# Kernel tuning notes

Measured on AMD Instinct MI355X. Metric: run time of the kernel, lower is better.

Reference implementation:

```python
import jax, jax.numpy as jnp
import numpy as np

B, S, EMBED, DK, DV, M = 8, 1024, 1024, 512, 512, 64


def setup_inputs() -> dict:
    key = jax.random.key(0)
    ks = jax.random.split(key, 9)
    query_in = jax.random.normal(ks[0], (B, S, EMBED), dtype=jnp.float32)
    key_in = jax.random.normal(ks[1], (B, S, EMBED), dtype=jnp.float32)
    value_in = jax.random.normal(ks[2], (B, S, EMBED), dtype=jnp.float32)
    lim = 1.0 / np.sqrt(EMBED)  # nn.Linear default init range
    u = lambda k, shape: jax.random.uniform(k, shape, minval=-lim, maxval=lim, dtype=jnp.float32)
    return {
        'query_in': query_in, 'key_in': key_in, 'value_in': value_in,
        'Wq': u(ks[3], (DK, EMBED)), 'bq': u(ks[4], (DK,)),
        'Wk': u(ks[5], (DK, EMBED)), 'bk': u(ks[6], (DK,)),
        'Wv': u(ks[7], (DV, EMBED)), 'bv': u(ks[8], (DV,)),
    }


def _select_landmarks(k_proj, m):
    # Original code runs recursive RLS sampling (random, host-side) over the m
    # segment-rows of key.reshape(B, m, seg, d) and gathers m of them back,
    # then flattens to (B, S, d). We use a deterministic data-dependent
    # selection (rows ranked by squared norm) with identical gather structure.
    Bb, Ss, d = k_proj.shape
    seg = Ss // m
    kr = k_proj.reshape(Bb, m, seg, d)
    scores = jnp.sum(kr * kr, axis=(2, 3))                      # [B, m]
    idx = jnp.argsort(-scores, axis=1)                          # [B, m]
    land = jnp.take_along_axis(kr, idx[:, :, None, None], axis=1)
    return land.reshape(Bb, Ss, d)                              # [B, S, d]


def reference(query_in, key_in, value_in, Wq, bq, Wk, bk, Wv, bv):
    scaling = DK ** -0.25  # 1/sqrt(sqrt(d_k)), applied to both q and k
    q = (jnp.einsum('bse,de->bsd', query_in, Wq) + bq) * scaling
    k = (jnp.einsum('bse,de->bsd', key_in, Wk) + bk) * scaling
    v = jnp.einsum('bse,de->bsd', value_in, Wv) + bv

    kl = _select_landmarks(k, M)                                # [B, S, DK]
    # is_decoder_self_attn is hard-coded True upstream -> q_landmarks = q,
    # so kernel_2 == kernel_1.
    kernel_1 = jax.nn.softmax(jnp.einsum('bqd,bkd->bqk', q, kl), axis=-1)
    kernel_2 = kernel_1
    kernel_3 = jax.nn.softmax(jnp.einsum('bqd,bkd->bqk', q, k), axis=-1)

    k2_inv = jnp.linalg.pinv(kernel_2)                          # [B, S, S] batched SVD
    out = jnp.einsum('bqk,bkd->bqd', jnp.einsum('bqm,bmk->bqk', kernel_1, k2_inv),
                     jnp.einsum('bqk,bkd->bqd', kernel_3, v))
    # dropout is identity in eval mode
    return out
```

## Files before the change

### kernel.cpp

```cpp
#include <hip/hip_runtime.h>
#include <hip/hip_bf16.h>

#define SS   1024
#define DKK  512

typedef __hip_bfloat16 bf16;
typedef __attribute__((ext_vector_type(8))) short s16x8;
typedef __attribute__((ext_vector_type(8))) unsigned short u16x8;
typedef __attribute__((ext_vector_type(4))) float f32x4;

#define WS_W(z)  ((48ull << 20) + ((size_t)(z) << 20))
#define WS_ST    (51ull << 20)
#define WS_Q     (52ull << 20)
#define WS_K     (60ull << 20)
#define WS_VT    (68ull << 20)
#define WS_LG    (0ull)

__device__ __forceinline__ void async_ld16(const void* g, void* s) {
  __builtin_amdgcn_global_load_lds(
      (const __attribute__((address_space(1))) void*)g,
      (__attribute__((address_space(3))) void*)s, 16, 0, 0);
}

__device__ __forceinline__ unsigned short f2bfu(float f) {
  return __builtin_bit_cast(unsigned short, __float2bfloat16(f));
}
__device__ __forceinline__ float bfu2f(unsigned short u) {
  unsigned int i = ((unsigned int)u) << 16;
  return __builtin_bit_cast(float, i);
}

__global__ __launch_bounds__(256)
void convert_w(const float* __restrict__ w0, const float* __restrict__ w1,
               const float* __restrict__ w2, char* __restrict__ ws)
{
  const int bx = blockIdx.x;
  const int z = bx >> 8, local = bx & 255;
  const float* src = (z == 0) ? w0 : (z == 1) ? w1 : w2;
  unsigned short* dst = (unsigned short*)(ws + WS_W(z));
  const int i = local * 2048 + threadIdx.x * 8;
  const float4* s = (const float4*)(src + i);
  float4 a = s[0], b = s[1];
  ushort4 o0, o1;
  o0.x = f2bfu(a.x); o0.y = f2bfu(a.y); o0.z = f2bfu(a.z); o0.w = f2bfu(a.w);
  o1.x = f2bfu(b.x); o1.y = f2bfu(b.y); o1.z = f2bfu(b.z); o1.w = f2bfu(b.w);
  ((ushort4*)(dst + i))[0] = o0;
  ((ushort4*)(dst + i))[1] = o1;
}

template<int BM, int K, int LDA, int LDB>
__device__ __forceinline__ void gemm_core(const bf16* __restrict__ A,
                                          const bf16* __restrict__ Bw,
                                          int bm, int bn,
                                          short* As, short* Bs, f32x4* acc)
{
  constexpr int MI = BM / 32;
  constexpr int AR = BM / 4;
  const int tid  = threadIdx.x;
  const int lane = tid & 63;
  const int wave = tid >> 6;
  const int l8   = lane >> 3;
  const int kch  = ((lane & 7) ^ l8) * 8;
  const bf16* ag = A  + (size_t)(bm * BM + wave * AR + l8) * LDA + kch;
  const bf16* bg = Bw + (size_t)(bn * 128 + wave * 32 + l8) * LDB + kch;
  short* AsW = As + wave * AR * 64;
  short* BsW = Bs + wave * 32 * 64;
  const int waveM = wave >> 1, waveN = wave & 1;
  const int l16  = lane & 15;
  const int quad = lane >> 4;
  const int xr   = l16 & 7;

  #pragma unroll
  for (int t = 0; t < MI * 4; ++t)
    #pragma unroll
    for (int r = 0; r < 4; ++r) acc[t][r] = 0.0f;

  for (int kt = 0; kt < K / 64; ++kt) {
    #pragma unroll
    for (int j = 0; j < AR / 8; ++j) async_ld16(ag + (size_t)j * 8 * LDA, AsW + j * 8 * 64);
    #pragma unroll
    for (int j = 0; j < 4; ++j)      async_ld16(bg + (size_t)j * 8 * LDB, BsW + j * 8 * 64);
    ag += 64; bg += 64;
    __syncthreads();
    #pragma unroll
    for (int ks = 0; ks < 2; ++ks) {
      s16x8 af[MI], bfv[4];
      #pragma unroll
      for (int mi = 0; mi < MI; ++mi) {
        const int row  = waveM * (BM / 2) + mi * 16 + l16;
        const int slot = (ks * 4 + quad) ^ xr;
        af[mi] = *(const s16x8*)&As[row * 64 + slot * 8];
      }
      #pragma unroll
      for (int ni = 0; ni < 4; ++ni) {
        const int row  = waveN * 64 + ni * 16 + l16;
        const int slot = (ks * 4 + quad) ^ xr;
        bfv[ni] = *(const s16x8*)&Bs[row * 64 + slot * 8];
      }
      #pragma unroll
      for (int mi = 0; mi < MI; ++mi)
        #pragma unroll
        for (int ni = 0; ni < 4; ++ni)
          acc[mi * 4 + ni] = __builtin_amdgcn_mfma_f32_16x16x32_bf16(
              af[mi], bfv[ni], acc[mi * 4 + ni], 0, 0, 0);
    }
    __syncthreads();
  }
}

template<int K, int LDA, int LDB>
__device__ __forceinline__ void gemm_core_f32a(const float* __restrict__ A,
                                               const bf16* __restrict__ Bw,
                                               int bm, int bn,
                                               short* As, short* Bs, f32x4* acc)
{
  const int tid  = threadIdx.x;
  const int lane = tid & 63;
  const int wave = tid >> 6;
  const int l8   = lane >> 3;
  const int kch  = ((lane & 7) ^ l8) * 8;
  const bf16* bg = Bw + (size_t)(bn * 256 + wave * 64 + l8) * LDB + kch;
  short* BsW = Bs + wave * 64 * 64;
  const int arow = tid >> 3;
  const int ag8  = tid & 7;
  const int slotA = (ag8 ^ (arow & 7)) * 8;
  const float* ag = A + (size_t)(bm * 64 + arow) * LDA + ag8 * 8;
  const int waveM = wave >> 1, waveN = wave & 1;
  const int l16  = lane & 15;
  const int quad = lane >> 4;
  const int xr   = l16 & 7;

  #pragma unroll
  for (int t = 0; t < 16; ++t)
    #pragma unroll
    for (int r = 0; r < 4; ++r) acc[t][r] = 0.0f;

  for (int kt = 0; kt < K / 64; ++kt) {
    #pragma unroll
    for (int j = 0; j < 8; ++j) async_ld16(bg + (size_t)j * 8 * LDB, BsW + j * 8 * 64);
    bg += 64;
    #pragma unroll
    for (int p = 0; p < 2; ++p) {
      const float4* s = (const float4*)(ag + (size_t)p * 32 * LDA);
      float4 a = s[0], b = s[1];
      u16x8 v;
      v[0] = f2bfu(a.x); v[1] = f2bfu(a.y); v[2] = f2bfu(a.z); v[3] = f2bfu(a.w);
      v[4] = f2bfu(b.x); v[5] = f2bfu(b.y); v[6] = f2bfu(b.z); v[7] = f2bfu(b.w);
      *(u16x8*)&As[(p * 32 + arow) * 64 + slotA] = v;
    }
    ag += 64;
    __syncthreads();
    #pragma unroll
    for (int ks = 0; ks < 2; ++ks) {
      s16x8 af[2], bfv[8];
      #pragma unroll
      for (int mi = 0; mi < 2; ++mi) {
        const int row  = waveM * 32 + mi * 16 + l16;
        const int slot = (ks * 4 + quad) ^ xr;
        af[mi] = *(const s16x8*)&As[row * 64 + slot * 8];
      }
      #pragma unroll
      for (int ni = 0; ni < 8; ++ni) {
        const int row  = waveN * 128 + ni * 16 + l16;
        const int slot = (ks * 4 + quad) ^ xr;
        bfv[ni] = *(const s16x8*)&Bs[row * 64 + slot * 8];
      }
      #pragma unroll
      for (int mi = 0; mi < 2; ++mi)
        #pragma unroll
        for (int ni = 0; ni < 8; ++ni)
          acc[mi * 8 + ni] = __builtin_amdgcn_mfma_f32_16x16x32_bf16(
              af[mi], bfv[ni], acc[mi * 8 + ni], 0, 0, 0);
    }
    __syncthreads();
  }
}

__global__ __launch_bounds__(256, 3)
void proj_kernel(const float* __restrict__ Xq, const float* __restrict__ Xk,
                 const float* __restrict__ Xv, const bf16* __restrict__ W0,
                 const float* __restrict__ bq, const float* __restrict__ bk,
                 const float* __restrict__ bv,
                 bf16* __restrict__ qo, bf16* __restrict__ ko,
                 bf16* __restrict__ vT, float qscale)
{
  __shared__ __align__(16) short As[64 * 64];
  __shared__ __align__(16) short Bs[256 * 64];
  const int id   = blockIdx.x;
  const int xcd  = id & 7;
  const int s    = id >> 3;
  const int bn   = s & 1;
  const int pair = (s >> 1) * 8 + xcd;
  const int bm   = pair & 127;
  const int z    = pair >> 7;
  const float* A  = (z == 0) ? Xq : (z == 1) ? Xk : Xv;
  const bf16*  Bw = W0 + ((size_t)z << 19);
  const float* bias = (z == 0) ? bq : (z == 1) ? bk : bv;
  f32x4 acc[16];
  gemm_core_f32a<1024, 1024, 1024>(A, Bw, bm, bn, As, Bs, acc);

  const int lane = threadIdx.x & 63;
  const int wave = threadIdx.x >> 6;
  const int waveM = wave >> 1, waveN = wave & 1;
  const int l16 = lane & 15, quad = lane >> 4;
  const int row0 = bm * 64 + waveM * 32;
  const int col0 = bn * 256 + waveN * 128;
  const float sc = (z == 0) ? qscale : 1.0f;
  bf16* C = (z == 0) ? qo : ko;
  #pragma unroll
  for (int ni = 0; ni < 8; ++ni) {
    const int col = col0 + ni * 16 + l16;
    const float bb = bias[col];
    #pragma unroll
    for (int mi = 0; mi < 2; ++mi)
      #pragma unroll
      for (int r = 0; r < 4; ++r) {
        const int row = row0 + mi * 16 + quad * 4 + r;
        const float v = acc[mi * 8 + ni][r] + bb;
        if (z == 2)
          vT[((size_t)(row >> 10) * DKK + col) * SS + (row & (SS - 1))] =
              __float2bfloat16(v);
        else
          C[(size_t)row * DKK + col] = __float2bfloat16(v * sc);
      }
  }
}

__global__ __launch_bounds__(256, 4)
void scores_kernel(const bf16* __restrict__ q, const bf16* __restrict__ k,
                   bf16* __restrict__ lgB, float* __restrict__ stats)
{
  __shared__ __align__(16) short As[64 * 64];
  __shared__ __align__(16) short Bs[128 * 64];
  const int z = blockIdx.z;
  const int bn = blockIdx.x, bm = blockIdx.y;
  f32x4 acc[8];
  gemm_core<64, 512, 512, 512>(q + (size_t)z * SS * DKK, k + (size_t)z * SS * DKK,
                               bm, bn, As, Bs, acc);

  const int lane = threadIdx.x & 63;
  const int wave = threadIdx.x >> 6;
  const int waveM = wave >> 1, waveN = wave & 1;
  const int l16 = lane & 15, quad = lane >> 4;
  const int row0 = bm * 64 + waveM * 32;
  const int col0 = bn * 128 + waveN * 64;
  bf16* C = lgB + (size_t)z * SS * SS;
  #pragma unroll
  for (int ni = 0; ni < 4; ++ni) {
    const int col = col0 + ni * 16 + l16;
    #pragma unroll
    for (int mi = 0; mi < 2; ++mi)
      #pragma unroll
      for (int r = 0; r < 4; ++r) {
        const int row = row0 + mi * 16 + quad * 4 + r;
        C[(size_t)row * SS + col] = __float2bfloat16(acc[mi * 4 + ni][r]);
      }
  }
  const int chunk = bn * 2 + waveN;
  #pragma unroll
  for (int mi = 0; mi < 2; ++mi)
    #pragma unroll
    for (int r = 0; r < 4; ++r) {
      float xr4[4];
      float m = -1e30f;
      #pragma unroll
      for (int ni = 0; ni < 4; ++ni) {
        xr4[ni] = bfu2f(f2bfu(acc[mi * 4 + ni][r]));
        m = fmaxf(m, xr4[ni]);
      }
      #pragma unroll
      for (int msk = 1; msk < 16; msk <<= 1) m = fmaxf(m, __shfl_xor(m, msk));
      float e = 0.f;
      #pragma unroll
      for (int ni = 0; ni < 4; ++ni) e += __expf(xr4[ni] - m);
      #pragma unroll
      for (int msk = 1; msk < 16; msk <<= 1) e += __shfl_xor(e, msk);
      if (l16 == 0) {
        const int row = row0 + mi * 16 + quad * 4 + r;
        float2 mr; mr.x = m; mr.y = e;
        *(float2*)&stats[(((size_t)z * SS + row) * 16 + chunk) * 2] = mr;
      }
    }
}

__device__ __forceinline__ void gemm_core_pv(const unsigned short* __restrict__ lg,
                                             const bf16* __restrict__ vT,
                                             int bm, int bn,
                                             const float* Ml, const float* Rl,
                                             short* As, short* Bs, f32x4* acc)
{
  const int tid  = threadIdx.x;
  const int lane = tid & 63;
  const int wave = tid >> 6;
  const int l8   = lane >> 3;
  const int kch  = ((lane & 7) ^ l8) * 8;
  const bf16* bg = vT + (size_t)(bn * 128 + wave * 32 + l8) * 1024 + kch;
  short* BsW = Bs + wave * 32 * 64;
  const int arow = tid >> 3;
  const int ag8  = tid & 7;
  const int slotA = (ag8 ^ (arow & 7)) * 8;
  const unsigned short* ag = lg + (size_t)(bm * 64 + arow) * 1024 + ag8 * 8;
  const int waveM = wave >> 1, waveN = wave & 1;
  const int l16  = lane & 15;
  const int quad = lane >> 4;
  const int xr   = l16 & 7;

  #pragma unroll
  for (int t = 0; t < 8; ++t)
    #pragma unroll
    for (int r = 0; r < 4; ++r) acc[t][r] = 0.0f;

  for (int kt = 0; kt < 16; ++kt) {
    #pragma unroll
    for (int j = 0; j < 4; ++j) async_ld16(bg + (size_t)j * 8 * 1024, BsW + j * 8 * 64);
    bg += 64;
    #pragma unroll
    for (int p = 0; p < 2; ++p) {
      const int rl = p * 32 + arow;
      u16x8 u = *(const u16x8*)(ag + (size_t)p * 32 * 1024);
      const float M = Ml[rl], R = Rl[rl];
      u16x8 v;
      #pragma unroll
      for (int j = 0; j < 8; ++j)
        v[j] = f2bfu(__expf(bfu2f((unsigned short)u[j]) - M) * R);
      *(u16x8*)&As[rl * 64 + slotA] = v;
    }
    ag += 64;
    __syncthreads();
    #pragma unroll
    for (int ks = 0; ks < 2; ++ks) {
      s16x8 af[2], bfv[4];
      #pragma unroll
      for (int mi = 0; mi < 2; ++mi) {
        const int row  = waveM * 32 + mi * 16 + l16;
        const int slot = (ks * 4 + quad) ^ xr;
        af[mi] = *(const s16x8*)&As[row * 64 + slot * 8];
      }
      #pragma unroll
      for (int ni = 0; ni < 4; ++ni) {
        const int row  = waveN * 64 + ni * 16 + l16;
        const int slot = (ks * 4 + quad) ^ xr;
        bfv[ni] = *(const s16x8*)&Bs[row * 64 + slot * 8];
      }
      #pragma unroll
      for (int mi = 0; mi < 2; ++mi)
        #pragma unroll
        for (int ni = 0; ni < 4; ++ni)
          acc[mi * 4 + ni] = __builtin_amdgcn_mfma_f32_16x16x32_bf16(
              af[mi], bfv[ni], acc[mi * 4 + ni], 0, 0, 0);
    }
    __syncthreads();
  }
}

__global__ __launch_bounds__(256, 4)
void pv_kernel(const unsigned short* __restrict__ lgB, const bf16* __restrict__ vT,
               const float* __restrict__ stats, float* __restrict__ out)
{
  __shared__ __align__(16) short As[64 * 64];
  __shared__ __align__(16) short Bs[128 * 64];
  __shared__ float Ml[64], Rl[64];
  const int z = blockIdx.z;
  const int bn = blockIdx.x, bm = blockIdx.y;
  const int tid = threadIdx.x;

  if (tid < 64) {
    const int row = bm * 64 + tid;
    const float* st = stats + ((size_t)z * SS + row) * 32;
    float mc[16], lc[16];
    float M = -1e30f;
    #pragma unroll
    for (int c = 0; c < 16; ++c) {
      mc[c] = st[c * 2]; lc[c] = st[c * 2 + 1];
      M = fmaxf(M, mc[c]);
    }
    float L = 0.f;
    #pragma unroll
    for (int c = 0; c < 16; ++c) L += __expf(mc[c] - M) * lc[c];
    Ml[tid] = M; Rl[tid] = 1.0f / L;
  }
  __syncthreads();

  f32x4 acc[8];
  gemm_core_pv(lgB + (size_t)z * SS * SS, vT + (size_t)z * DKK * SS,
               bm, bn, Ml, Rl, As, Bs, acc);

  const int lane = tid & 63;
  const int wave = tid >> 6;
  const int waveM = wave >> 1, waveN = wave & 1;
  const int l16 = lane & 15, quad = lane >> 4;
  const int row0 = bm * 64 + waveM * 32;
  const int col0 = bn * 128 + waveN * 64;
  float* C = out + (size_t)z * SS * DKK;
  #pragma unroll
  for (int ni = 0; ni < 4; ++ni) {
    const int col = col0 + ni * 16 + l16;
    #pragma unroll
    for (int mi = 0; mi < 2; ++mi)
      #pragma unroll
      for (int r = 0; r < 4; ++r) {
        const int row = row0 + mi * 16 + quad * 4 + r;
        C[(size_t)row * DKK + col] = acc[mi * 4 + ni][r];
      }
  }
}

extern "C" void kernel_launch(void* const* d_in, const int* in_sizes, int n_in,
                              void* d_out, int out_size, void* d_ws, size_t ws_size,
                              hipStream_t stream)
{
  char* ws = (char*)d_ws;
  bf16*  W0   = (bf16*)(ws + WS_W(0));
  float* stat = (float*)(ws + WS_ST);
  bf16*  q    = (bf16*)(ws + WS_Q);
  bf16*  kk   = (bf16*)(ws + WS_K);
  bf16*  vT   = (bf16*)(ws + WS_VT);
  bf16*  lgB  = (bf16*)(ws + WS_LG);

  const float qscale = 0.044194173824159216f;

  dim3 blk(256, 1, 1);
  hipLaunchKernelGGL(convert_w, dim3(768), blk, 0, stream,
                     (const float*)d_in[3], (const float*)d_in[5],
                     (const float*)d_in[7], ws);
  hipLaunchKernelGGL(proj_kernel, dim3(768, 1, 1), blk, 0, stream,
                     (const float*)d_in[0], (const float*)d_in[1],
                     (const float*)d_in[2], W0,
                     (const float*)d_in[4], (const float*)d_in[6],
                     (const float*)d_in[8], q, kk, vT, qscale);
  hipLaunchKernelGGL(scores_kernel, dim3(8, 16, 8), blk, 0, stream,
                     q, kk, lgB, stat);
  hipLaunchKernelGGL(pv_kernel, dim3(4, 16, 8), blk, 0, stream,
                     (const unsigned short*)lgB, vT, stat, (float*)d_out);
}
```

Before: 219.9 us.

## Double-buffer LDS tiles with prefetch in proj, scores and pv GEMM kernels

Replaces the single-buffered GEMM cores with double-buffered LDS pipelines. The next K-tile's async global-to-LDS loads and register prefetches are issued before the current tile's MFMA work, using explicit vmcnt waits and barriers. The aim is to overlap global memory latency with matrix math. It also flattens the scores and pv grids to 1D with the batch index in the low bits, which spreads batches across XCDs, and it lowers occupancy bounds to fit the doubled shared memory, trading waves per CU for overlap.

```diff
diff --git a/kernel.cpp b/kernel.cpp
--- a/kernel.cpp
+++ b/kernel.cpp
@@ -29,6 +29,10 @@
   unsigned int i = ((unsigned int)u) << 16;
   return __builtin_bit_cast(float, i);
 }
+
+#define FENCE() __builtin_amdgcn_sched_barrier(0)
+#define LGKM0() asm volatile("s_waitcnt lgkmcnt(0)" ::: "memory")
+#define BAR()   __builtin_amdgcn_s_barrier()
 
 __global__ __launch_bounds__(256)
 void convert_w(const float* __restrict__ w0, const float* __restrict__ w1,
@@ -48,135 +52,7 @@
   ((ushort4*)(dst + i))[1] = o1;
 }
 
-template<int BM, int K, int LDA, int LDB>
-__device__ __forceinline__ void gemm_core(const bf16* __restrict__ A,
-                                          const bf16* __restrict__ Bw,
-                                          int bm, int bn,
-                                          short* As, short* Bs, f32x4* acc)
-{
-  constexpr int MI = BM / 32;
-  constexpr int AR = BM / 4;
-  const int tid  = threadIdx.x;
-  const int lane = tid & 63;
-  const int wave = tid >> 6;
-  const int l8   = lane >> 3;
-  const int kch  = ((lane & 7) ^ l8) * 8;
-  const bf16* ag = A  + (size_t)(bm * BM + wave * AR + l8) * LDA + kch;
-  const bf16* bg = Bw + (size_t)(bn * 128 + wave * 32 + l8) * LDB + kch;
-  short* AsW = As + wave * AR * 64;
-  short* BsW = Bs + wave * 32 * 64;
-  const int waveM = wave >> 1, waveN = wave & 1;
-  const int l16  = lane & 15;
-  const int quad = lane >> 4;
-  const int xr   = l16 & 7;
-
-  #pragma unroll
-  for (int t = 0; t < MI * 4; ++t)
-    #pragma unroll
-    for (int r = 0; r < 4; ++r) acc[t][r] = 0.0f;
-
-  for (int kt = 0; kt < K / 64; ++kt) {
-    #pragma unroll
-    for (int j = 0; j < AR / 8; ++j) async_ld16(ag + (size_t)j * 8 * LDA, AsW + j * 8 * 64);
-    #pragma unroll
-    for (int j = 0; j < 4; ++j)      async_ld16(bg + (size_t)j * 8 * LDB, BsW + j * 8 * 64);
-    ag += 64; bg += 64;
-    __syncthreads();
-    #pragma unroll
-    for (int ks = 0; ks < 2; ++ks) {
-      s16x8 af[MI], bfv[4];
-      #pragma unroll
-      for (int mi = 0; mi < MI; ++mi) {
-        const int row  = waveM * (BM / 2) + mi * 16 + l16;
-        const int slot = (ks * 4 + quad) ^ xr;
-        af[mi] = *(const s16x8*)&As[row * 64 + slot * 8];
-      }
-      #pragma unroll
-      for (int ni = 0; ni < 4; ++ni) {
-        const int row  = waveN * 64 + ni * 16 + l16;
-        const int slot = (ks * 4 + quad) ^ xr;
-        bfv[ni] = *(const s16x8*)&Bs[row * 64 + slot * 8];
-      }
-      #pragma unroll
-      for (int mi = 0; mi < MI; ++mi)
-        #pragma unroll
-        for (int ni = 0; ni < 4; ++ni)
-          acc[mi * 4 + ni] = __builtin_amdgcn_mfma_f32_16x16x32_bf16(
-              af[mi], bfv[ni], acc[mi * 4 + ni], 0, 0, 0);
-    }
-    __syncthreads();
-  }
-}
-
-template<int K, int LDA, int LDB>
-__device__ __forceinline__ void gemm_core_f32a(const float* __restrict__ A,
-                                               const bf16* __restrict__ Bw,
-                                               int bm, int bn,
-                                               short* As, short* Bs, f32x4* acc)
-{
-  const int tid  = threadIdx.x;
-  const int lane = tid & 63;
-  const int wave = tid >> 6;
-  const int l8   = lane >> 3;
-  const int kch  = ((lane & 7) ^ l8) * 8;
-  const bf16* bg = Bw + (size_t)(bn * 256 + wave * 64 + l8) * LDB + kch;
-  short* BsW = Bs + wave * 64 * 64;
-  const int arow = tid >> 3;
-  const int ag8  = tid & 7;
-  const int slotA = (ag8 ^ (arow & 7)) * 8;
-  const float* ag = A + (size_t)(bm * 64 + arow) * LDA + ag8 * 8;
-  const int waveM = wave >> 1, waveN = wave & 1;
-  const int l16  = lane & 15;
-  const int quad = lane >> 4;
-  const int xr   = l16 & 7;
-
-  #pragma unroll
-  for (int t = 0; t < 16; ++t)
-    #pragma unroll
-    for (int r = 0; r < 4; ++r) acc[t][r] = 0.0f;
-
-  for (int kt = 0; kt < K / 64; ++kt) {
-    #pragma unroll
-    for (int j = 0; j < 8; ++j) async_ld16(bg + (size_t)j * 8 * LDB, BsW + j * 8 * 64);
-    bg += 64;
-    #pragma unroll
-    for (int p = 0; p < 2; ++p) {
-      const float4* s = (const float4*)(ag + (size_t)p * 32 * LDA);
-      float4 a = s[0], b = s[1];
-      u16x8 v;
-      v[0] = f2bfu(a.x); v[1] = f2bfu(a.y); v[2] = f2bfu(a.z); v[3] = f2bfu(a.w);
-      v[4] = f2bfu(b.x); v[5] = f2bfu(b.y); v[6] = f2bfu(b.z); v[7] = f2bfu(b.w);
-      *(u16x8*)&As[(p * 32 + arow) * 64 + slotA] = v;
-    }
-    ag += 64;
-    __syncthreads();
-    #pragma unroll
-    for (int ks = 0; ks < 2; ++ks) {
-      s16x8 af[2], bfv[8];
-      #pragma unroll
-      for (int mi = 0; mi < 2; ++mi) {
-        const int row  = waveM * 32 + mi * 16 + l16;
-        const int slot = (ks * 4 + quad) ^ xr;
-        af[mi] = *(const s16x8*)&As[row * 64 + slot * 8];
-      }
-      #pragma unroll
-      for (int ni = 0; ni < 8; ++ni) {
-        const int row  = waveN * 128 + ni * 16 + l16;
-        const int slot = (ks * 4 + quad) ^ xr;
-        bfv[ni] = *(const s16x8*)&Bs[row * 64 + slot * 8];
-      }
-      #pragma unroll
-      for (int mi = 0; mi < 2; ++mi)
-        #pragma unroll
-        for (int ni = 0; ni < 8; ++ni)
-          acc[mi * 8 + ni] = __builtin_amdgcn_mfma_f32_16x16x32_bf16(
-              af[mi], bfv[ni], acc[mi * 8 + ni], 0, 0, 0);
-    }
-    __syncthreads();
-  }
-}
-
-__global__ __launch_bounds__(256, 3)
+__global__ __launch_bounds__(256, 2)
 void proj_kernel(const float* __restrict__ Xq, const float* __restrict__ Xk,
                  const float* __restrict__ Xv, const bf16* __restrict__ W0,
                  const float* __restrict__ bq, const float* __restrict__ bk,
@@ -184,8 +60,8 @@
                  bf16* __restrict__ qo, bf16* __restrict__ ko,
                  bf16* __restrict__ vT, float qscale)
 {
-  __shared__ __align__(16) short As[64 * 64];
-  __shared__ __align__(16) short Bs[256 * 64];
+  __shared__ __align__(16) short As[2][64 * 64];
+  __shared__ __align__(16) short Bs[2][256 * 64];
   const int id   = blockIdx.x;
   const int xcd  = id & 7;
   const int s    = id >> 3;
@@ -196,13 +72,107 @@
   const float* A  = (z == 0) ? Xq : (z == 1) ? Xk : Xv;
   const bf16*  Bw = W0 + ((size_t)z << 19);
   const float* bias = (z == 0) ? bq : (z == 1) ? bk : bv;
+
+  const int tid  = threadIdx.x;
+  const int lane = tid & 63;
+  const int wave = tid >> 6;
+  const int l8   = lane >> 3;
+  const int kch  = ((lane & 7) ^ l8) * 8;
+  const bf16* bg = Bw + (size_t)(bn * 256 + wave * 64 + l8) * 1024 + kch;
+  const int bsoff = wave * 64 * 64;
+  const int arow = tid >> 3;
+  const int ag8  = tid & 7;
+  const int slotA = (ag8 ^ (arow & 7)) * 8;
+  const float* ag = A + (size_t)(bm * 64 + arow) * 1024 + ag8 * 8;
+  const int waveM = wave >> 1, waveN = wave & 1;
+  const int l16  = lane & 15;
+  const int quad = lane >> 4;
+  const int xr   = l16 & 7;
+
   f32x4 acc[16];
-  gemm_core_f32a<1024, 1024, 1024>(A, Bw, bm, bn, As, Bs, acc);
-
-  const int lane = threadIdx.x & 63;
-  const int wave = threadIdx.x >> 6;
-  const int waveM = wave >> 1, waveN = wave & 1;
-  const int l16 = lane & 15, quad = lane >> 4;
+  #pragma unroll
+  for (int t = 0; t < 16; ++t)
+    #pragma unroll
+    for (int r = 0; r < 4; ++r) acc[t][r] = 0.0f;
+
+  float4 ca0 = ((const float4*)ag)[0];
+  float4 cb0 = ((const float4*)ag)[1];
+  float4 ca1 = ((const float4*)(ag + (size_t)32 * 1024))[0];
+  float4 cb1 = ((const float4*)(ag + (size_t)32 * 1024))[1];
+  {
+    u16x8 v;
+    v[0] = f2bfu(ca0.x); v[1] = f2bfu(ca0.y); v[2] = f2bfu(ca0.z); v[3] = f2bfu(ca0.w);
+    v[4] = f2bfu(cb0.x); v[5] = f2bfu(cb0.y); v[6] = f2bfu(cb0.z); v[7] = f2bfu(cb0.w);
+    *(u16x8*)&As[0][arow * 64 + slotA] = v;
+    v[0] = f2bfu(ca1.x); v[1] = f2bfu(ca1.y); v[2] = f2bfu(ca1.z); v[3] = f2bfu(ca1.w);
+    v[4] = f2bfu(cb1.x); v[5] = f2bfu(cb1.y); v[6] = f2bfu(cb1.z); v[7] = f2bfu(cb1.w);
+    *(u16x8*)&As[0][(32 + arow) * 64 + slotA] = v;
+  }
+  #pragma unroll
+  for (int j = 0; j < 8; ++j)
+    async_ld16(bg + (size_t)j * 8 * 1024, &Bs[0][bsoff + j * 8 * 64]);
+  const float* agi = ag + 64;
+  float4 na0 = ((const float4*)agi)[0];
+  float4 nb0 = ((const float4*)agi)[1];
+  float4 na1 = ((const float4*)(agi + (size_t)32 * 1024))[0];
+  float4 nb1 = ((const float4*)(agi + (size_t)32 * 1024))[1];
+  agi += 64;
+  const bf16* bgi = bg + 64;
+
+  for (int t = 0; t < 16; ++t) {
+    const int X = t & 1;
+    #pragma unroll
+    for (int j = 0; j < 8; ++j)
+      async_ld16(bgi + (size_t)j * 8 * 1024, &Bs[X ^ 1][bsoff + j * 8 * 64]);
+    if (t < 14) bgi += 64;
+    FENCE();
+    {
+      u16x8 v;
+      v[0] = f2bfu(na0.x); v[1] = f2bfu(na0.y); v[2] = f2bfu(na0.z); v[3] = f2bfu(na0.w);
+      v[4] = f2bfu(nb0.x); v[5] = f2bfu(nb0.y); v[6] = f2bfu(nb0.z); v[7] = f2bfu(nb0.w);
+      *(u16x8*)&As[X ^ 1][arow * 64 + slotA] = v;
+      v[0] = f2bfu(na1.x); v[1] = f2bfu(na1.y); v[2] = f2bfu(na1.z); v[3] = f2bfu(na1.w);
+      v[4] = f2bfu(nb1.x); v[5] = f2bfu(nb1.y); v[6] = f2bfu(nb1.z); v[7] = f2bfu(nb1.w);
+      *(u16x8*)&As[X ^ 1][(32 + arow) * 64 + slotA] = v;
+    }
+    na0 = ((const float4*)agi)[0];
+    nb0 = ((const float4*)agi)[1];
+    na1 = ((const float4*)(agi + (size_t)32 * 1024))[0];
+    nb1 = ((const float4*)(agi + (size_t)32 * 1024))[1];
+    if (t < 13) agi += 64;
+    FENCE();
+    asm volatile("s_waitcnt vmcnt(12)" ::: "memory");
+    LGKM0();
+    FENCE();
+    BAR();
+    FENCE();
+    #pragma unroll
+    for (int ks = 0; ks < 2; ++ks) {
+      s16x8 af[2], bfv[8];
+      #pragma unroll
+      for (int mi = 0; mi < 2; ++mi) {
+        const int row  = waveM * 32 + mi * 16 + l16;
+        const int slot = (ks * 4 + quad) ^ xr;
+        af[mi] = *(const s16x8*)&As[X][row * 64 + slot * 8];
+      }
+      #pragma unroll
+      for (int ni = 0; ni < 8; ++ni) {
+        const int row  = waveN * 128 + ni * 16 + l16;
+        const int slot = (ks * 4 + quad) ^ xr;
+        bfv[ni] = *(const s16x8*)&Bs[X][row * 64 + slot * 8];
+      }
+      #pragma unroll
+      for (int mi = 0; mi < 2; ++mi)
+        #pragma unroll
+        for (int ni = 0; ni < 8; ++ni)
+          acc[mi * 8 + ni] = __builtin_amdgcn_mfma_f32_16x16x32_bf16(
+              af[mi], bfv[ni], acc[mi * 8 + ni], 0, 0, 0);
+    }
+    FENCE();
+    BAR();
+    FENCE();
+  }
+
   const int row0 = bm * 64 + waveM * 32;
   const int col0 = bn * 256 + waveN * 128;
   const float sc = (z == 0) ? qscale : 1.0f;
@@ -226,22 +196,87 @@
   }
 }
 
-__global__ __launch_bounds__(256, 4)
+__global__ __launch_bounds__(256, 3)
 void scores_kernel(const bf16* __restrict__ q, const bf16* __restrict__ k,
                    bf16* __restrict__ lgB, float* __restrict__ stats)
 {
-  __shared__ __align__(16) short As[64 * 64];
-  __shared__ __align__(16) short Bs[128 * 64];
-  const int z = blockIdx.z;
-  const int bn = blockIdx.x, bm = blockIdx.y;
+  __shared__ __align__(16) short As[2][64 * 64];
+  __shared__ __align__(16) short Bs[2][128 * 64];
+  const int id = blockIdx.x;
+  const int z  = id & 7;
+  const int sx = id >> 3;
+  const int bm = sx & 15;
+  const int bn = sx >> 4;
+  const bf16* qz = q + (size_t)z * SS * DKK;
+  const bf16* kz = k + (size_t)z * SS * DKK;
+
+  const int tid  = threadIdx.x;
+  const int lane = tid & 63;
+  const int wave = tid >> 6;
+  const int l8   = lane >> 3;
+  const int kch  = ((lane & 7) ^ l8) * 8;
+  const bf16* ag = qz + (size_t)(bm * 64 + wave * 16 + l8) * 512 + kch;
+  const bf16* bg = kz + (size_t)(bn * 128 + wave * 32 + l8) * 512 + kch;
+  const int asoff = wave * 16 * 64;
+  const int bsoff = wave * 32 * 64;
+  const int waveM = wave >> 1, waveN = wave & 1;
+  const int l16  = lane & 15;
+  const int quad = lane >> 4;
+  const int xr   = l16 & 7;
+
   f32x4 acc[8];
-  gemm_core<64, 512, 512, 512>(q + (size_t)z * SS * DKK, k + (size_t)z * SS * DKK,
-                               bm, bn, As, Bs, acc);
-
-  const int lane = threadIdx.x & 63;
-  const int wave = threadIdx.x >> 6;
-  const int waveM = wave >> 1, waveN = wave & 1;
-  const int l16 = lane & 15, quad = lane >> 4;
+  #pragma unroll
+  for (int t = 0; t < 8; ++t)
+    #pragma unroll
+    for (int r = 0; r < 4; ++r) acc[t][r] = 0.0f;
+
+  #pragma unroll
+  for (int j = 0; j < 2; ++j) async_ld16(ag + (size_t)j * 8 * 512, &As[0][asoff + j * 8 * 64]);
+  #pragma unroll
+  for (int j = 0; j < 4; ++j) async_ld16(bg + (size_t)j * 8 * 512, &Bs[0][bsoff + j * 8 * 64]);
+  const bf16* agi = ag + 64;
+  const bf16* bgi = bg + 64;
+
+  for (int t = 0; t < 8; ++t) {
+    const int X = t & 1;
+    #pragma unroll
+    for (int j = 0; j < 2; ++j) async_ld16(agi + (size_t)j * 8 * 512, &As[X ^ 1][asoff + j * 8 * 64]);
+    #pragma unroll
+    for (int j = 0; j < 4; ++j) async_ld16(bgi + (size_t)j * 8 * 512, &Bs[X ^ 1][bsoff + j * 8 * 64]);
+    if (t < 6) { agi += 64; bgi += 64; }
+    FENCE();
+    asm volatile("s_waitcnt vmcnt(6)" ::: "memory");
+    LGKM0();
+    FENCE();
+    BAR();
+    FENCE();
+    #pragma unroll
+    for (int ks = 0; ks < 2; ++ks) {
+      s16x8 af[2], bfv[4];
+      #pragma unroll
+      for (int mi = 0; mi < 2; ++mi) {
+        const int row  = waveM * 32 + mi * 16 + l16;
+        const int slot = (ks * 4 + quad) ^ xr;
+        af[mi] = *(const s16x8*)&As[X][row * 64 + slot * 8];
+      }
+      #pragma unroll
+      for (int ni = 0; ni < 4; ++ni) {
+        const int row  = waveN * 64 + ni * 16 + l16;
+        const int slot = (ks * 4 + quad) ^ xr;
+        bfv[ni] = *(const s16x8*)&Bs[X][row * 64 + slot * 8];
+      }
+      #pragma unroll
+      for (int mi = 0; mi < 2; ++mi)
+        #pragma unroll
+        for (int ni = 0; ni < 4; ++ni)
+          acc[mi * 4 + ni] = __builtin_amdgcn_mfma_f32_16x16x32_bf16(
+              af[mi], bfv[ni], acc[mi * 4 + ni], 0, 0, 0);
+    }
+    FENCE();
+    BAR();
+    FENCE();
+  }
+
   const int row0 = bm * 64 + waveM * 32;
   const int col0 = bn * 128 + waveN * 64;
   bf16* C = lgB + (size_t)z * SS * SS;
@@ -283,19 +318,45 @@
     }
 }
 
-__device__ __forceinline__ void gemm_core_pv(const unsigned short* __restrict__ lg,
-                                             const bf16* __restrict__ vT,
-                                             int bm, int bn,
-                                             const float* Ml, const float* Rl,
-                                             short* As, short* Bs, f32x4* acc)
+__global__ __launch_bounds__(256, 3)
+void pv_kernel(const unsigned short* __restrict__ lgB, const bf16* __restrict__ vT,
+               const float* __restrict__ stats, float* __restrict__ out)
 {
-  const int tid  = threadIdx.x;
+  __shared__ __align__(16) short As[2][64 * 64];
+  __shared__ __align__(16) short Bs[2][128 * 64];
+  __shared__ float Ml[64], Rl[64];
+  const int id = blockIdx.x;
+  const int z  = id & 7;
+  const int sx = id >> 3;
+  const int bm = sx & 15;
+  const int bn = sx >> 4;
+  const int tid = threadIdx.x;
+
+  if (tid < 64) {
+    const int row = bm * 64 + tid;
+    const float* st = stats + ((size_t)z * SS + row) * 32;
+    float mc[16], lc[16];
+    float M = -1e30f;
+    #pragma unroll
+    for (int c = 0; c < 16; ++c) {
+      mc[c] = st[c * 2]; lc[c] = st[c * 2 + 1];
+      M = fmaxf(M, mc[c]);
+    }
+    float L = 0.f;
+    #pragma unroll
+    for (int c = 0; c < 16; ++c) L += __expf(mc[c] - M) * lc[c];
+    Ml[tid] = M; Rl[tid] = 1.0f / L;
+  }
+  __syncthreads();
+
+  const unsigned short* lg = lgB + (size_t)z * SS * SS;
+  const bf16* vz = vT + (size_t)z * DKK * SS;
   const int lane = tid & 63;
   const int wave = tid >> 6;
   const int l8   = lane >> 3;
   const int kch  = ((lane & 7) ^ l8) * 8;
-  const bf16* bg = vT + (size_t)(bn * 128 + wave * 32 + l8) * 1024 + kch;
-  short* BsW = Bs + wave * 32 * 64;
+  const bf16* bg = vz + (size_t)(bn * 128 + wave * 32 + l8) * 1024 + kch;
+  const int bsoff = wave * 32 * 64;
   const int arow = tid >> 3;
   const int ag8  = tid & 7;
   const int slotA = (ag8 ^ (arow & 7)) * 8;
@@ -305,28 +366,60 @@
   const int quad = lane >> 4;
   const int xr   = l16 & 7;
 
+  const float M0 = Ml[arow],      R0 = Rl[arow];
+  const float M1 = Ml[32 + arow], R1 = Rl[32 + arow];
+
+  f32x4 acc[8];
   #pragma unroll
   for (int t = 0; t < 8; ++t)
     #pragma unroll
     for (int r = 0; r < 4; ++r) acc[t][r] = 0.0f;
 
-  for (int kt = 0; kt < 16; ++kt) {
-    #pragma unroll
-    for (int j = 0; j < 4; ++j) async_ld16(bg + (size_t)j * 8 * 1024, BsW + j * 8 * 64);
-    bg += 64;
-    #pragma unroll
-    for (int p = 0; p < 2; ++p) {
-      const int rl = p * 32 + arow;
-      u16x8 u = *(const u16x8*)(ag + (size_t)p * 32 * 1024);
-      const float M = Ml[rl], R = Rl[rl];
+  u16x8 cu0 = *(const u16x8*)ag;
+  u16x8 cu1 = *(const u16x8*)(ag + (size_t)32 * 1024);
+  {
+    u16x8 v;
+    #pragma unroll
+    for (int j = 0; j < 8; ++j) v[j] = f2bfu(__expf(bfu2f((unsigned short)cu0[j]) - M0) * R0);
+    *(u16x8*)&As[0][arow * 64 + slotA] = v;
+    #pragma unroll
+    for (int j = 0; j < 8; ++j) v[j] = f2bfu(__expf(bfu2f((unsigned short)cu1[j]) - M1) * R1);
+    *(u16x8*)&As[0][(32 + arow) * 64 + slotA] = v;
+  }
+  #pragma unroll
+  for (int j = 0; j < 4; ++j)
+    async_ld16(bg + (size_t)j * 8 * 1024, &Bs[0][bsoff + j * 8 * 64]);
+  const unsigned short* agi = ag + 64;
+  u16x8 nu0 = *(const u16x8*)agi;
+  u16x8 nu1 = *(const u16x8*)(agi + (size_t)32 * 1024);
+  agi += 64;
+  const bf16* bgi = bg + 64;
+
+  for (int t = 0; t < 16; ++t) {
+    const int X = t & 1;
+    #pragma unroll
+    for (int j = 0; j < 4; ++j)
+      async_ld16(bgi + (size_t)j * 8 * 1024, &Bs[X ^ 1][bsoff + j * 8 * 64]);
+    if (t < 14) bgi += 64;
+    FENCE();
+    {
       u16x8 v;
       #pragma unroll
-      for (int j = 0; j < 8; ++j)
-        v[j] = f2bfu(__expf(bfu2f((unsigned short)u[j]) - M) * R);
-      *(u16x8*)&As[rl * 64 + slotA] = v;
-    }
-    ag += 64;
-    __syncthreads();
+      for (int j = 0; j < 8; ++j) v[j] = f2bfu(__expf(bfu2f((unsigned short)nu0[j]) - M0) * R0);
+      *(u16x8*)&As[X ^ 1][arow * 64 + slotA] = v;
+      #pragma unroll
+      for (int j = 0; j < 8; ++j) v[j] = f2bfu(__expf(bfu2f((unsigned short)nu1[j]) - M1) * R1);
+      *(u16x8*)&As[X ^ 1][(32 + arow) * 64 + slotA] = v;
+    }
+    nu0 = *(const u16x8*)agi;
+    nu1 = *(const u16x8*)(agi + (size_t)32 * 1024);
+    if (t < 13) agi += 64;
+    FENCE();
+    asm volatile("s_waitcnt vmcnt(6)" ::: "memory");
+    LGKM0();
+    FENCE();
+    BAR();
+    FENCE();
     #pragma unroll
     for (int ks = 0; ks < 2; ++ks) {
       s16x8 af[2], bfv[4];
@@ -334,13 +427,13 @@
       for (int mi = 0; mi < 2; ++mi) {
         const int row  = waveM * 32 + mi * 16 + l16;
         const int slot = (ks * 4 + quad) ^ xr;
-        af[mi] = *(const s16x8*)&As[row * 64 + slot * 8];
+        af[mi] = *(const s16x8*)&As[X][row * 64 + slot * 8];
       }
       #pragma unroll
       for (int ni = 0; ni < 4; ++ni) {
         const int row  = waveN * 64 + ni * 16 + l16;
         const int slot = (ks * 4 + quad) ^ xr;
-        bfv[ni] = *(const s16x8*)&Bs[row * 64 + slot * 8];
+        bfv[ni] = *(const s16x8*)&Bs[X][row * 64 + slot * 8];
       }
       #pragma unroll
       for (int mi = 0; mi < 2; ++mi)
@@ -349,46 +442,11 @@
           acc[mi * 4 + ni] = __builtin_amdgcn_mfma_f32_16x16x32_bf16(
               af[mi], bfv[ni], acc[mi * 4 + ni], 0, 0, 0);
     }
-    __syncthreads();
-  }
-}
-
-__global__ __launch_bounds__(256, 4)
-void pv_kernel(const unsigned short* __restrict__ lgB, const bf16* __restrict__ vT,
-               const float* __restrict__ stats, float* __restrict__ out)
-{
-  __shared__ __align__(16) short As[64 * 64];
-  __shared__ __align__(16) short Bs[128 * 64];
-  __shared__ float Ml[64], Rl[64];
-  const int z = blockIdx.z;
-  const int bn = blockIdx.x, bm = blockIdx.y;
-  const int tid = threadIdx.x;
-
-  if (tid < 64) {
-    const int row = bm * 64 + tid;
-    const float* st = stats + ((size_t)z * SS + row) * 32;
-    float mc[16], lc[16];
-    float M = -1e30f;
-    #pragma unroll
-    for (int c = 0; c < 16; ++c) {
-      mc[c] = st[c * 2]; lc[c] = st[c * 2 + 1];
-      M = fmaxf(M, mc[c]);
-    }
-    float L = 0.f;
-    #pragma unroll
-    for (int c = 0; c < 16; ++c) L += __expf(mc[c] - M) * lc[c];
-    Ml[tid] = M; Rl[tid] = 1.0f / L;
-  }
-  __syncthreads();
-
-  f32x4 acc[8];
-  gemm_core_pv(lgB + (size_t)z * SS * SS, vT + (size_t)z * DKK * SS,
-               bm, bn, Ml, Rl, As, Bs, acc);
-
-  const int lane = tid & 63;
-  const int wave = tid >> 6;
-  const int waveM = wave >> 1, waveN = wave & 1;
-  const int l16 = lane & 15, quad = lane >> 4;
+    FENCE();
+    BAR();
+    FENCE();
+  }
+
   const int row0 = bm * 64 + waveM * 32;
   const int col0 = bn * 128 + waveN * 64;
   float* C = out + (size_t)z * SS * DKK;
@@ -428,8 +486,8 @@
                      (const float*)d_in[2], W0,
                      (const float*)d_in[4], (const float*)d_in[6],
                      (const float*)d_in[8], q, kk, vT, qscale);
-  hipLaunchKernelGGL(scores_kernel, dim3(8, 16, 8), blk, 0, stream,
+  hipLaunchKernelGGL(scores_kernel, dim3(1024, 1, 1), blk, 0, stream,
                      q, kk, lgB, stat);
-  hipLaunchKernelGGL(pv_kernel, dim3(4, 16, 8), blk, 0, stream,
+  hipLaunchKernelGGL(pv_kernel, dim3(512, 1, 1), blk, 0, stream,
                      (const unsigned short*)lgB, vT, stat, (float*)d_out);
 }
```

Measured after the change: 245.7 us. 11.7% more time.
